# Performance work log

Hardware: AMD Instinct MI355X
Metric: run time of the kernel (lower is better)

Reference implementation:

```python
import jax, jax.numpy as jnp
import numpy as np
from jax import lax

DISCOUNT = 0.99
NORMALIZE = True
EPS = 1e-9


def setup_inputs() -> dict:
    key = jax.random.key(0)
    k1, k2 = jax.random.split(key)
    B, T = 4096, 8192
    rewards = jax.random.normal(k1, (B, T), dtype=jnp.float32)
    done_flags = (jax.random.uniform(k2, (B, T)) < 0.01).astype(jnp.float32)
    return {"rewards": rewards, "done_flags": done_flags}


def _episode_returns(rewards, done_flags):
    # reverse-time recurrence: r_t = rew_t + gamma * r_{t+1} * (1 - done_t)
    rw = jnp.moveaxis(rewards, -1, 0)      # [T, B]
    dn = jnp.moveaxis(done_flags, -1, 0)   # [T, B]

    def step(carry, xs):
        r, d = xs
        ret = r + DISCOUNT * carry * (1.0 - d)
        return ret, ret

    # init carry = 0 makes the last step reduce to returns[-1] = rewards[-1]
    _, rets = lax.scan(step, jnp.zeros_like(rw[0]), (rw, dn), reverse=True)
    returns = jnp.moveaxis(rets, 0, -1)    # [B, T]

    if NORMALIZE:
        # torch: (returns - returns.mean()) / (returns.std(dim=-1) + 1e-9)
        # global mean, per-trajectory std (unbiased, matching torch default)
        std = jnp.std(returns, axis=-1, ddof=1, keepdims=True)
        returns = (returns - jnp.mean(returns)) / (std + EPS)
    return returns


def reference(rewards, done_flags):
    return _episode_returns(rewards, done_flags)
```

## Files before the change

kernel.cpp:

```cpp
#include <hip/hip_runtime.h>
#include <math.h>

#define TLEN   8192
#define BROWS  4096
#define NT     256
#define TILE   2048
#define CHUNK  8
#define NTILES (TLEN / TILE)
#define GAMMA  0.99f
#define EPSN   1e-9

__device__ __forceinline__ void stash(float* lds, int e0, float4 v) {
  const int w = e0 + (e0 >> 3);
  lds[w + 0] = v.x;
  lds[w + 1] = v.y;
  lds[w + 2] = v.z;
  lds[w + 3] = v.w;
}

__global__ __launch_bounds__(NT) void er_scan(const float* __restrict__ rew,
                                              const float* __restrict__ don,
                                              float* __restrict__ out,
                                              double* __restrict__ rowSum,
                                              float* __restrict__ rowInv) {
  __shared__ float  ldsR[TILE + TILE / 8];
  __shared__ float  ldsD[TILE + TILE / 8];
  __shared__ float  wgA[4], wgP[4];
  __shared__ double red[8];

  const int row  = blockIdx.x;
  const int tid  = threadIdx.x;
  const int lane = tid & 63;
  const int wv   = tid >> 6;
  const size_t rbase = (size_t)row * TLEN;

  const float4* gr = (const float4*)(rew + rbase);
  const float4* gd = (const float4*)(don + rbase);

  float4 pr0, pr1, pd0, pd1;
  {
    const int f = (NTILES - 1) * (TILE / 4);
    pr0 = gr[f + tid];      pr1 = gr[f + NT + tid];
    pd0 = gd[f + tid];      pd1 = gd[f + NT + tid];
  }
  stash(ldsR, 4 * tid, pr0);  stash(ldsR, 1024 + 4 * tid, pr1);
  stash(ldsD, 4 * tid, pd0);  stash(ldsD, 1024 + 4 * tid, pd1);
  __syncthreads();

  double accS = 0.0, accQ = 0.0;
  float  tc = 0.f;

  for (int k = NTILES - 1; k >= 0; --k) {
    const bool more = (k > 0);
    if (more) {
      const int f = (k - 1) * (TILE / 4);
      pr0 = gr[f + tid];    pr1 = gr[f + NT + tid];
      pd0 = gd[f + tid];    pd1 = gd[f + NT + tid];
    }

    float rv[CHUNK], cv[CHUNK];
    const int wbase = 9 * tid;
#pragma unroll
    for (int j = 0; j < CHUNK; ++j) rv[j] = ldsR[wbase + j];
#pragma unroll
    for (int j = 0; j < CHUNK; ++j) cv[j] = GAMMA - GAMMA * ldsD[wbase + j];

    float A = 0.f, P = 1.f;
#pragma unroll
    for (int j = CHUNK - 1; j >= 0; --j) {
      A = fmaf(cv[j], A, rv[j]);
      P *= cv[j];
      rv[j] = A;
      cv[j] = P;
    }

    float sA = A, sP = P;
#pragma unroll
    for (int d = 1; d < 64; d <<= 1) {
      const float tA = __shfl_down(sA, d);
      const float tP = __shfl_down(sP, d);
      if (lane + d < 64) { sA = fmaf(sP, tA, sA); sP *= tP; }
    }
    if (lane == 0) { wgA[wv] = sA; wgP[wv] = sP; }
    __syncthreads();

    float wc = tc;
#pragma unroll
    for (int j = 3; j >= 1; --j) {
      const float nw = fmaf(wgP[j], wc, wgA[j]);
      wc = (j > wv) ? nw : wc;
    }
    float tcn = tc;
#pragma unroll
    for (int j = 3; j >= 0; --j) tcn = fmaf(wgP[j], tcn, wgA[j]);

    float eA = __shfl_down(sA, 1);
    float eP = __shfl_down(sP, 1);
    if (lane == 63) { eA = 0.f; eP = 1.f; }
    const float carry = fmaf(eP, wc, eA);

    if (more) {
      stash(ldsR, 4 * tid, pr0);  stash(ldsR, 1024 + 4 * tid, pr1);
      stash(ldsD, 4 * tid, pd0);  stash(ldsD, 1024 + 4 * tid, pd1);
    }

    float fsum = 0.f, fsq = 0.f;
    float o[CHUNK];
#pragma unroll
    for (int j = 0; j < CHUNK; ++j) {
      const float r = fmaf(cv[j], carry, rv[j]);
      o[j] = r;
      fsum += r;
      fsq  = fmaf(r, r, fsq);
    }
    float4* go = (float4*)(out + rbase + (size_t)k * TILE + (size_t)tid * CHUNK);
    go[0] = make_float4(o[0], o[1], o[2], o[3]);
    go[1] = make_float4(o[4], o[5], o[6], o[7]);
    accS += (double)fsum;
    accQ += (double)fsq;
    tc = tcn;

    if (more) __syncthreads();
  }

  double ds = accS, dq = accQ;
#pragma unroll
  for (int d = 32; d >= 1; d >>= 1) {
    ds += __shfl_down(ds, d);
    dq += __shfl_down(dq, d);
  }
  if (lane == 0) { red[wv] = ds; red[4 + wv] = dq; }
  __syncthreads();
  if (tid == 0) {
    const double s = red[0] + red[1] + red[2] + red[3];
    const double q = red[4] + red[5] + red[6] + red[7];
    rowSum[row] = s;
    double var = (q - s * s / (double)TLEN) / (double)(TLEN - 1);
    if (var < 0.0) var = 0.0;
    rowInv[row] = (float)(1.0 / (sqrt(var) + EPSN));
  }
}

__global__ __launch_bounds__(256) void er_mean(const double* __restrict__ rowSum,
                                               float* __restrict__ meanPtr) {
  const int tid = threadIdx.x;
  double s = 0.0;
  for (int i = tid; i < BROWS; i += 256) s += rowSum[i];
#pragma unroll
  for (int d = 32; d >= 1; d >>= 1) s += __shfl_down(s, d);
  __shared__ double red[4];
  const int lane = tid & 63, wv = tid >> 6;
  if (lane == 0) red[wv] = s;
  __syncthreads();
  if (tid == 0) {
    const double t = red[0] + red[1] + red[2] + red[3];
    *meanPtr = (float)(t / ((double)BROWS * (double)TLEN));
  }
}

__global__ __launch_bounds__(256) void er_norm(float* __restrict__ out,
                                               const float* __restrict__ rowInv,
                                               const float* __restrict__ meanPtr) {
  const int row = blockIdx.x;
  const float mean = *meanPtr;
  const float inv  = rowInv[row];
  float4* o4 = (float4*)(out + (size_t)row * TLEN);
#pragma unroll
  for (int i = threadIdx.x; i < TLEN / 4; i += 256) {
    float4 v = o4[i];
    v.x = (v.x - mean) * inv;
    v.y = (v.y - mean) * inv;
    v.z = (v.z - mean) * inv;
    v.w = (v.w - mean) * inv;
    o4[i] = v;
  }
}

extern "C" void kernel_launch(void* const* d_in, const int* in_sizes, int n_in,
                              void* d_out, int out_size, void* d_ws, size_t ws_size,
                              hipStream_t stream) {
  const float* rew = (const float*)d_in[0];
  const float* don = (const float*)d_in[1];
  float* out = (float*)d_out;

  double* rowSum  = (double*)d_ws;
  float*  rowInv  = (float*)((char*)d_ws + BROWS * 8);
  float*  meanPtr = (float*)((char*)d_ws + BROWS * 8 + BROWS * 4);

  er_scan<<<BROWS, NT, 0, stream>>>(rew, don, out, rowSum, rowInv);
  er_mean<<<1, 256, 0, stream>>>(rowSum, meanPtr);
  er_norm<<<BROWS, 256, 0, stream>>>(out, rowInv, meanPtr);
}
```

Measured before the change: 351.7 us.

## Load scan inputs directly into registers, drop LDS staging; grid-stride norm with nontemporal stores

The scan kernel now has each thread load its own 8 contiguous elements as two float4 vectors straight from global memory into registers, prefetching the next tile in registers. This removes the LDS stash/reload round trip and one barrier per tile. The per-wave partials are indexed by tile so the old trailing barrier is no longer needed. The normalize kernel becomes a grid-stride loop over 2048 blocks and uses nontemporal stores. Per-thread loads are now 32-byte strided rather than fully coalesced across lanes, which may reduce load efficiency.

```diff
diff --git a/kernel.cpp b/kernel.cpp
--- a/kernel.cpp
+++ b/kernel.cpp
@@ -10,22 +10,15 @@
 #define GAMMA  0.99f
 #define EPSN   1e-9
 
-__device__ __forceinline__ void stash(float* lds, int e0, float4 v) {
-  const int w = e0 + (e0 >> 3);
-  lds[w + 0] = v.x;
-  lds[w + 1] = v.y;
-  lds[w + 2] = v.z;
-  lds[w + 3] = v.w;
-}
+typedef float f4 __attribute__((ext_vector_type(4)));
 
 __global__ __launch_bounds__(NT) void er_scan(const float* __restrict__ rew,
                                               const float* __restrict__ don,
                                               float* __restrict__ out,
                                               double* __restrict__ rowSum,
                                               float* __restrict__ rowInv) {
-  __shared__ float  ldsR[TILE + TILE / 8];
-  __shared__ float  ldsD[TILE + TILE / 8];
-  __shared__ float  wgA[4], wgP[4];
+  __shared__ float  wgA[NTILES][4];
+  __shared__ float  wgP[NTILES][4];
   __shared__ double red[8];
 
   const int row  = blockIdx.x;
@@ -34,36 +27,39 @@
   const int wv   = tid >> 6;
   const size_t rbase = (size_t)row * TLEN;
 
-  const float4* gr = (const float4*)(rew + rbase);
-  const float4* gd = (const float4*)(don + rbase);
+  const f4* gr = (const f4*)(rew + rbase);
+  const f4* gd = (const f4*)(don + rbase);
 
-  float4 pr0, pr1, pd0, pd1;
+  f4 r0, r1, d0, d1;
   {
-    const int f = (NTILES - 1) * (TILE / 4);
-    pr0 = gr[f + tid];      pr1 = gr[f + NT + tid];
-    pd0 = gd[f + tid];      pd1 = gd[f + NT + tid];
+    const int f = (NTILES - 1) * (TILE / 4) + 2 * tid;
+    r0 = gr[f]; r1 = gr[f + 1];
+    d0 = gd[f]; d1 = gd[f + 1];
   }
-  stash(ldsR, 4 * tid, pr0);  stash(ldsR, 1024 + 4 * tid, pr1);
-  stash(ldsD, 4 * tid, pd0);  stash(ldsD, 1024 + 4 * tid, pd1);
-  __syncthreads();
 
   double accS = 0.0, accQ = 0.0;
   float  tc = 0.f;
 
   for (int k = NTILES - 1; k >= 0; --k) {
     const bool more = (k > 0);
+    f4 pr0, pr1, pd0, pd1;
     if (more) {
-      const int f = (k - 1) * (TILE / 4);
-      pr0 = gr[f + tid];    pr1 = gr[f + NT + tid];
-      pd0 = gd[f + tid];    pd1 = gd[f + NT + tid];
+      const int f = (k - 1) * (TILE / 4) + 2 * tid;
+      pr0 = gr[f]; pr1 = gr[f + 1];
+      pd0 = gd[f]; pd1 = gd[f + 1];
     }
 
     float rv[CHUNK], cv[CHUNK];
-    const int wbase = 9 * tid;
-#pragma unroll
-    for (int j = 0; j < CHUNK; ++j) rv[j] = ldsR[wbase + j];
-#pragma unroll
-    for (int j = 0; j < CHUNK; ++j) cv[j] = GAMMA - GAMMA * ldsD[wbase + j];
+    rv[0] = r0.x; rv[1] = r0.y; rv[2] = r0.z; rv[3] = r0.w;
+    rv[4] = r1.x; rv[5] = r1.y; rv[6] = r1.z; rv[7] = r1.w;
+    cv[0] = fmaf(-GAMMA, d0.x, GAMMA);
+    cv[1] = fmaf(-GAMMA, d0.y, GAMMA);
+    cv[2] = fmaf(-GAMMA, d0.z, GAMMA);
+    cv[3] = fmaf(-GAMMA, d0.w, GAMMA);
+    cv[4] = fmaf(-GAMMA, d1.x, GAMMA);
+    cv[5] = fmaf(-GAMMA, d1.y, GAMMA);
+    cv[6] = fmaf(-GAMMA, d1.z, GAMMA);
+    cv[7] = fmaf(-GAMMA, d1.w, GAMMA);
 
     float A = 0.f, P = 1.f;
 #pragma unroll
@@ -81,28 +77,23 @@
       const float tP = __shfl_down(sP, d);
       if (lane + d < 64) { sA = fmaf(sP, tA, sA); sP *= tP; }
     }
-    if (lane == 0) { wgA[wv] = sA; wgP[wv] = sP; }
+    if (lane == 0) { wgA[k][wv] = sA; wgP[k][wv] = sP; }
     __syncthreads();
 
     float wc = tc;
 #pragma unroll
     for (int j = 3; j >= 1; --j) {
-      const float nw = fmaf(wgP[j], wc, wgA[j]);
+      const float nw = fmaf(wgP[k][j], wc, wgA[k][j]);
       wc = (j > wv) ? nw : wc;
     }
     float tcn = tc;
 #pragma unroll
-    for (int j = 3; j >= 0; --j) tcn = fmaf(wgP[j], tcn, wgA[j]);
+    for (int j = 3; j >= 0; --j) tcn = fmaf(wgP[k][j], tcn, wgA[k][j]);
 
     float eA = __shfl_down(sA, 1);
     float eP = __shfl_down(sP, 1);
     if (lane == 63) { eA = 0.f; eP = 1.f; }
     const float carry = fmaf(eP, wc, eA);
-
-    if (more) {
-      stash(ldsR, 4 * tid, pr0);  stash(ldsR, 1024 + 4 * tid, pr1);
-      stash(ldsD, 4 * tid, pd0);  stash(ldsD, 1024 + 4 * tid, pd1);
-    }
 
     float fsum = 0.f, fsq = 0.f;
     float o[CHUNK];
@@ -113,14 +104,16 @@
       fsum += r;
       fsq  = fmaf(r, r, fsq);
     }
-    float4* go = (float4*)(out + rbase + (size_t)k * TILE + (size_t)tid * CHUNK);
-    go[0] = make_float4(o[0], o[1], o[2], o[3]);
-    go[1] = make_float4(o[4], o[5], o[6], o[7]);
+    f4* go = (f4*)(out + rbase + (size_t)k * TILE + (size_t)tid * CHUNK);
+    f4 o0; o0.x = o[0]; o0.y = o[1]; o0.z = o[2]; o0.w = o[3];
+    f4 o1; o1.x = o[4]; o1.y = o[5]; o1.z = o[6]; o1.w = o[7];
+    go[0] = o0;
+    go[1] = o1;
     accS += (double)fsum;
     accQ += (double)fsq;
     tc = tcn;
 
-    if (more) __syncthreads();
+    if (more) { r0 = pr0; r1 = pr1; d0 = pd0; d1 = pd1; }
   }
 
   double ds = accS, dq = accQ;
@@ -158,21 +151,23 @@
   }
 }
 
+#define K3_BLOCKS 2048
 __global__ __launch_bounds__(256) void er_norm(float* __restrict__ out,
                                                const float* __restrict__ rowInv,
                                                const float* __restrict__ meanPtr) {
-  const int row = blockIdx.x;
   const float mean = *meanPtr;
-  const float inv  = rowInv[row];
-  float4* o4 = (float4*)(out + (size_t)row * TLEN);
-#pragma unroll
-  for (int i = threadIdx.x; i < TLEN / 4; i += 256) {
-    float4 v = o4[i];
+  const unsigned total4 = (unsigned)BROWS * (TLEN / 4);
+  const unsigned stride = K3_BLOCKS * 256;
+  f4* o4 = (f4*)out;
+  for (unsigned i = blockIdx.x * 256 + threadIdx.x; i < total4; i += stride) {
+    const int row = (int)(i >> 11);
+    const float inv = rowInv[row];
+    f4 v = o4[i];
     v.x = (v.x - mean) * inv;
     v.y = (v.y - mean) * inv;
     v.z = (v.z - mean) * inv;
     v.w = (v.w - mean) * inv;
-    o4[i] = v;
+    __builtin_nontemporal_store(v, o4 + i);
   }
 }
 
@@ -189,5 +184,5 @@
 
   er_scan<<<BROWS, NT, 0, stream>>>(rew, don, out, rowSum, rowInv);
   er_mean<<<1, 256, 0, stream>>>(rowSum, meanPtr);
-  er_norm<<<BROWS, 256, 0, stream>>>(out, rowInv, meanPtr);
+  er_norm<<<K3_BLOCKS, 256, 0, stream>>>(out, rowInv, meanPtr);
 }
```

Result: slower. 361.0 us (+2.6%).
